# Kernel optimization log

Measured on AMD Instinct MI355X. Metric: run time of the kernel, lower is better.

The kernel has to match this reference:

```python
import jax, jax.numpy as jnp
import numpy as np

N = 512            # hidden_state
BATCH = 64
L = 8192           # seq_len; kernel_max_size == L so kernel length = L
MIN_DELTA = 1e-3
MAX_DELTA = 0.1


def _hippo(n):
    idx = np.arange(n)
    init = np.sqrt(2.0 * idx + 1.0)
    H = np.outer(init, init)           # init @ init.T
    H = np.tril(H)                      # zero strict upper triangle
    H[idx, idx] -= idx                  # diag -= arange(N)
    return (-H).astype(np.float32)


def setup_inputs() -> dict:
    key = jax.random.key(0)
    kx, kb, kc, kd = jax.random.split(key, 4)
    X = jax.random.normal(kx, (BATCH, L), dtype=jnp.float32)
    A = jnp.asarray(_hippo(N))                                   # [N,N] HiPPO init
    Bm = jax.random.normal(kb, (N, 1), dtype=jnp.float32) * (1.0 / N) ** 0.5
    C = jax.random.normal(kc, (1, N), dtype=jnp.float32)
    D = jnp.ones((1,), dtype=jnp.float32)
    log_delta = jax.random.uniform(
        kd, (1,), dtype=jnp.float32,
        minval=np.log(MIN_DELTA), maxval=np.log(MAX_DELTA))
    return {"X": X, "A": A, "Bm": Bm, "C": C, "D": D, "log_delta": log_delta}


def reference(X, A, Bm, C, D, log_delta):
    # delta = exp(clamp(log_delta, log(min), log(max)))
    delta = jnp.exp(jnp.clip(log_delta, jnp.log(MIN_DELTA), jnp.log(MAX_DELTA)))[0]
    # bilinear (Tustin) discretization
    I = jnp.eye(N, dtype=X.dtype)
    A1 = I - delta * 0.5 * A
    A2 = I + delta * 0.5 * A
    Ad = jnp.linalg.solve(A1, A2)           # [N,N]
    Bd = jnp.linalg.solve(A1, delta * Bm)   # [N,1]

    # kernel k[t] = C @ Ad^t @ Bd, t = 0..L-1 (sequential scan)
    def step(v, _):
        return Ad @ v, (C @ v)[0, 0]
    _, k = jax.lax.scan(step, Bd, None, length=L)  # [L]

    # FFT linear (causal) convolution, truncated to L
    end = L + L - 1
    Xd = jnp.fft.rfft(X, n=end, axis=-1)      # [B, F]
    Kd = jnp.fft.rfft(k, n=end)               # [F]
    y = jnp.fft.irfft(Xd * Kd, n=end, axis=-1)[..., :L]
    return y + D * X
```

## Files before the change

kernel.cpp:

```cpp
#include <hip/hip_runtime.h>

#define N 512
#define L 8192

#define LOG_MIN -6.907755278982137f
#define LOG_MAX -2.302585092994046f

typedef __attribute__((ext_vector_type(8))) short short8;
typedef __attribute__((ext_vector_type(4))) float f4;
typedef __attribute__((ext_vector_type(4))) unsigned u4;

__device__ __forceinline__ float get_delta(const float* logd) {
  float ld = logd[0];
  ld = fminf(fmaxf(ld, LOG_MIN), LOG_MAX);
  return expf(ld);
}
__device__ __forceinline__ unsigned short f2bf(float x) {
  union { float f; unsigned int u; } c; c.f = x;
  unsigned int u = c.u;
  u += 0x7FFFu + ((u >> 16) & 1u);
  return (unsigned short)(u >> 16);
}
__device__ __forceinline__ unsigned int pack2(unsigned short a, unsigned short b) {
  return (unsigned int)a | ((unsigned int)b << 16);
}

__device__ __forceinline__ void wts4(float* p, f4 v) {
  asm volatile("global_store_dwordx4 %0, %1, off sc0 sc1"
               :: "v"(p), "v"(v) : "memory");
}
__device__ __forceinline__ void wts4u(unsigned* p, u4 v) {
  asm volatile("global_store_dwordx4 %0, %1, off sc0 sc1"
               :: "v"(p), "v"(v) : "memory");
}
__device__ __forceinline__ void ast(float* p, float v) {
  __hip_atomic_store(p, v, __ATOMIC_RELAXED, __HIP_MEMORY_SCOPE_AGENT);
}

#define NB 152u

__device__ __forceinline__ void gsync(unsigned* bar, int p, int b) {
  asm volatile("s_waitcnt vmcnt(0)" ::: "memory");
  __syncthreads();
  if (threadIdx.x == 0) {
    unsigned* base = bar + p * 128;
    __hip_atomic_fetch_add(base + (b & 7) * 16, 1u, __ATOMIC_RELAXED,
                           __HIP_MEMORY_SCOPE_AGENT);
    unsigned s;
    do {
      s = 0;
#pragma unroll
      for (int i = 0; i < 8; ++i)
        s += __hip_atomic_load(base + i * 16, __ATOMIC_RELAXED,
                               __HIP_MEMORY_SCOPE_AGENT);
      if (s < NB) __builtin_amdgcn_s_sleep(2);
    } while (s < NB);
  }
  __syncthreads();
}


__device__ void diag64(const float* __restrict__ A, float h,
                       float* __restrict__ Xi, int blk, int tid, float* sm) {
  float* Ash = sm;
  float* xs  = sm + 4160;
  float* dinv = sm + 8320;
  int i0 = blk * 64;
  int r = tid >> 2, c0 = (tid & 3) * 16;
#pragma unroll
  for (int q = 0; q < 16; q += 4) {
    f4 v = *(const f4*)(A + (size_t)(i0 + r) * N + i0 + c0 + q);
    Ash[r * 65 + c0 + q] = v.x; Ash[r * 65 + c0 + q + 1] = v.y;
    Ash[r * 65 + c0 + q + 2] = v.z; Ash[r * 65 + c0 + q + 3] = v.w;
  }
  for (int i = tid; i < 4160; i += 256) xs[i] = 0.f;
  __syncthreads();
  if (tid < 64) dinv[tid] = 1.f / (1.f - h * Ash[tid * 65 + tid]);
  __syncthreads();
  int t = tid >> 2, sub = tid & 3;
  for (int rr = 0; rr < 64; ++rr) {
    if (t <= rr) {
      float s = 0.f;
      for (int k = t + sub; k < rr; k += 4) s += Ash[rr * 65 + k] * xs[k * 65 + t];
      s += __shfl_xor(s, 1, 64);
      s += __shfl_xor(s, 2, 64);
      if (sub == 0)
        xs[rr * 65 + t] = (((rr == t) ? 1.f : 0.f) + h * s) * dinv[rr];
    }
  }
  __syncthreads();
#pragma unroll
  for (int q = 0; q < 16; q += 4) {
    f4 v = {xs[r * 65 + c0 + q], xs[r * 65 + c0 + q + 1],
            xs[r * 65 + c0 + q + 2], xs[r * 65 + c0 + q + 3]};
    wts4(Xi + (size_t)(i0 + r) * N + i0 + c0 + q, v);
  }
}

__device__ void lvl64_fused(const float* __restrict__ A, float* __restrict__ Xi,
                            float h, int g, int tid, float* sm) {
  float* X11s = sm;
  float* Us   = sm + 4160;
  int b11 = 128 * g, b22 = 128 * g + 64;
  int r = tid >> 2, c0 = (tid & 3) * 16;
#pragma unroll
  for (int q = 0; q < 16; q += 4) {
    f4 v = *(const f4*)(Xi + (size_t)(b11 + r) * N + b11 + c0 + q);
    X11s[r * 65 + c0 + q] = v.x; X11s[r * 65 + c0 + q + 1] = v.y;
    X11s[r * 65 + c0 + q + 2] = v.z; X11s[r * 65 + c0 + q + 3] = v.w;
  }
  f4 aR[16];
#pragma unroll
  for (int t = 0; t < 16; ++t)
    aR[t] = *(const f4*)(A + (size_t)(b22 + r) * N + b11 + 4 * t);
  __syncthreads();
  float u[16];
#pragma unroll
  for (int j = 0; j < 16; ++j) u[j] = 0.f;
#pragma unroll 4
  for (int k4 = 0; k4 < 16; ++k4) {
    float av[4] = {aR[k4].x, aR[k4].y, aR[k4].z, aR[k4].w};
#pragma unroll
    for (int s = 0; s < 4; ++s) {
      int k = 4 * k4 + s;
      float aa = av[s];
#pragma unroll
      for (int j = 0; j < 16; j += 4) {
        f4 xv = *(const f4*)&X11s[k * 65 + c0 + j];
        u[j] += aa * xv.x; u[j + 1] += aa * xv.y;
        u[j + 2] += aa * xv.z; u[j + 3] += aa * xv.w;
      }
    }
  }
  f4 xR[16];
#pragma unroll
  for (int t = 0; t < 16; ++t)
    xR[t] = *(const f4*)(Xi + (size_t)(b22 + r) * N + b22 + 4 * t);
#pragma unroll
  for (int j = 0; j < 16; ++j) Us[r * 65 + c0 + j] = u[j];
  __syncthreads();
  float x[16];
#pragma unroll
  for (int j = 0; j < 16; ++j) x[j] = 0.f;
#pragma unroll 4
  for (int k4 = 0; k4 < 16; ++k4) {
    float av[4] = {xR[k4].x, xR[k4].y, xR[k4].z, xR[k4].w};
#pragma unroll
    for (int s = 0; s < 4; ++s) {
      int k = 4 * k4 + s;
      float aa = av[s];
#pragma unroll
      for (int j = 0; j < 16; j += 4) {
        f4 xv = *(const f4*)&Us[k * 65 + c0 + j];
        x[j] += aa * xv.x; x[j + 1] += aa * xv.y;
        x[j + 2] += aa * xv.z; x[j + 3] += aa * xv.w;
      }
    }
  }
#pragma unroll
  for (int j = 0; j < 16; j += 4) {
    f4 v = {h * x[j], h * x[j + 1], h * x[j + 2], h * x[j + 3]};
    wts4(&Xi[(size_t)(b22 + r) * N + b11 + c0 + j], v);
  }
}

template <int NT>
__device__ void gemm32t(const float* __restrict__ A_, int lda,
                        const float* __restrict__ B_, int ldb,
                        float* __restrict__ C_, int ldc,
                        int bi, int bj, float alpha, int tid, float* sm) {
  float* As = sm;
  float* Bs = sm + 1056;
  int lr = tid >> 3, lc = (tid & 7) * 4;
  const float* ap = A_ + (size_t)(bi * 32 + lr) * lda + lc;
  const float* bp = B_ + (size_t)lr * ldb + bj * 32 + lc;
  f4 aR[NT], bR[NT];
#pragma unroll
  for (int t = 0; t < NT; ++t) {
    aR[t] = *(const f4*)(ap + 32 * t);
    bR[t] = *(const f4*)(bp + (size_t)(32 * t) * ldb);
  }
  float acc[4] = {0.f, 0.f, 0.f, 0.f};
#pragma unroll
  for (int t = 0; t < NT; ++t) {
    As[lr * 33 + lc] = aR[t].x; As[lr * 33 + lc + 1] = aR[t].y;
    As[lr * 33 + lc + 2] = aR[t].z; As[lr * 33 + lc + 3] = aR[t].w;
    *(f4*)&Bs[lr * 36 + lc] = bR[t];
    __syncthreads();
#pragma unroll
    for (int kk = 0; kk < 32; ++kk) {
      float a = As[lr * 33 + kk];
      f4 bb = *(const f4*)&Bs[kk * 36 + lc];
      acc[0] += a * bb.x; acc[1] += a * bb.y;
      acc[2] += a * bb.z; acc[3] += a * bb.w;
    }
    __syncthreads();
  }
  f4 o = {alpha * acc[0], alpha * acc[1], alpha * acc[2], alpha * acc[3]};
  wts4(&C_[(size_t)(bi * 32 + lr) * ldc + bj * 32 + lc], o);
}

__device__ void sq32(const float* __restrict__ P, float* __restrict__ Q,
                     int bi, int bj, int first, int tid, float* sm) {
  float* As = sm;
  float* Bs = sm + 1056;
  int lr = tid >> 3, lc = (tid & 7) * 4;
  int nk = bi - bj + 1;
  int kb0 = bj * 32;
  int arow = bi * 32 + lr;
  const float* ap = P + (size_t)arow * N + lc;
  const float* bp = P + bj * 32 + lc;
  f4 aR[16], bR[16];
#pragma unroll
  for (int t = 0; t < 16; ++t) {
    if (t < nk) {
      int kt = kb0 + 32 * t;
      aR[t] = *(const f4*)(ap + kt);
      bR[t] = *(const f4*)(bp + (size_t)(kt + lr) * N);
    }
  }
  float acc[4] = {0.f, 0.f, 0.f, 0.f};
#pragma unroll
  for (int t = 0; t < 16; ++t) {
    if (t < nk) {
      int kb = kb0 + 32 * t;
      float a4[4] = {aR[t].x, aR[t].y, aR[t].z, aR[t].w};
      float b4[4] = {bR[t].x, bR[t].y, bR[t].z, bR[t].w};
      if (first) {
#pragma unroll
        for (int j = 0; j < 4; ++j) {
          a4[j] = 2.f * a4[j] - ((arow == kb + lc + j) ? 1.f : 0.f);
          b4[j] = 2.f * b4[j] - ((kb + lr == bj * 32 + lc + j) ? 1.f : 0.f);
        }
      }
      As[lr * 33 + lc] = a4[0]; As[lr * 33 + lc + 1] = a4[1];
      As[lr * 33 + lc + 2] = a4[2]; As[lr * 33 + lc + 3] = a4[3];
      f4 bv = {b4[0], b4[1], b4[2], b4[3]};
      *(f4*)&Bs[lr * 36 + lc] = bv;
      __syncthreads();
#pragma unroll
      for (int kk = 0; kk < 32; ++kk) {
        float a = As[lr * 33 + kk];
        f4 bb = *(const f4*)&Bs[kk * 36 + lc];
        acc[0] += a * bb.x; acc[1] += a * bb.y;
        acc[2] += a * bb.z; acc[3] += a * bb.w;
      }
      __syncthreads();
    }
  }
  f4 o = {acc[0], acc[1], acc[2], acc[3]};
  wts4(&Q[(size_t)(bi * 32 + lr) * N + bj * 32 + lc], o);
}

__device__ void vstep_g(const float* __restrict__ P, float* __restrict__ Vtr,
                        int base, int first, int bi, int tid, float* sm) {
  float* As = sm;
  float* Bs = sm + 1056;
  int lr = tid >> 3, lc = (tid & 7) * 4;
  int cq = tid >> 3, n4 = (tid & 7) * 4;
  int nk = bi + 1;
  const float* ap = P + (size_t)(bi * 32 + lr) * N + lc;
  f4 aR[16];
#pragma unroll
  for (int t = 0; t < 16; ++t)
    if (t < nk) aR[t] = *(const f4*)(ap + 32 * t);
  int ncj = (base > 32) ? 2 : 1;
  for (int cj = 0; cj < ncj; ++cj) {
    int crow = cj * 32 + lr;
    int cok = (crow < base);
    const float* bp = Vtr + (size_t)crow * N + lc;
    f4 bR[16];
#pragma unroll
    for (int t = 0; t < 16; ++t)
      if (t < nk) bR[t] = cok ? *(const f4*)(bp + 32 * t) : (f4){0.f, 0.f, 0.f, 0.f};
    float acc[4] = {0.f, 0.f, 0.f, 0.f};
#pragma unroll
    for (int t = 0; t < 16; ++t) {
      if (t < nk) {
        int kb = 32 * t;
        float a4[4] = {aR[t].x, aR[t].y, aR[t].z, aR[t].w};
        if (first) {
#pragma unroll
          for (int j = 0; j < 4; ++j)
            a4[j] = 2.f * a4[j] - ((bi * 32 + lr == kb + lc + j) ? 1.f : 0.f);
        }
        As[lr * 33 + lc] = a4[0]; As[lr * 33 + lc + 1] = a4[1];
        As[lr * 33 + lc + 2] = a4[2]; As[lr * 33 + lc + 3] = a4[3];
        Bs[lr * 33 + lc] = bR[t].x; Bs[lr * 33 + lc + 1] = bR[t].y;
        Bs[lr * 33 + lc + 2] = bR[t].z; Bs[lr * 33 + lc + 3] = bR[t].w;
        __syncthreads();
#pragma unroll
        for (int kk = 0; kk < 32; ++kk) {
          float b = Bs[cq * 33 + kk];
          acc[0] += As[(n4 + 0) * 33 + kk] * b;
          acc[1] += As[(n4 + 1) * 33 + kk] * b;
          acc[2] += As[(n4 + 2) * 33 + kk] * b;
          acc[3] += As[(n4 + 3) * 33 + kk] * b;
        }
        __syncthreads();
      }
    }
    int c = cj * 32 + cq;
    if (c < base) {
      f4 o = {acc[0], acc[1], acc[2], acc[3]};
      wts4(&Vtr[(size_t)(base + c) * N + bi * 32 + n4], o);
    }
    if (cj + 1 < ncj) __syncthreads();
  }
}

__device__ void wstep_g(const float* __restrict__ P, float* __restrict__ W,
                        int base, int cj, int tid, float* sm) {
  float* As = sm;
  float* Bs = sm + 1056;
  int lr = tid >> 3, lc = (tid & 7) * 4;
  int kb0 = cj * 32, nk = 16 - cj;
  int qok = (lr < base);
  const float* ap = W + (size_t)lr * N + lc;
  const float* bp = P + cj * 32 + lc;
  f4 aR[16], bR[16];
#pragma unroll
  for (int t = 0; t < 16; ++t) {
    if (t < nk) {
      int kt = kb0 + 32 * t;
      aR[t] = qok ? *(const f4*)(ap + kt) : (f4){0.f, 0.f, 0.f, 0.f};
      bR[t] = *(const f4*)(bp + (size_t)(kt + lr) * N);
    }
  }
  float acc[4] = {0.f, 0.f, 0.f, 0.f};
#pragma unroll
  for (int t = 0; t < 16; ++t) {
    if (t < nk) {
      As[lr * 33 + lc] = aR[t].x; As[lr * 33 + lc + 1] = aR[t].y;
      As[lr * 33 + lc + 2] = aR[t].z; As[lr * 33 + lc + 3] = aR[t].w;
      *(f4*)&Bs[lr * 36 + lc] = bR[t];
      __syncthreads();
#pragma unroll
      for (int kk = 0; kk < 32; ++kk) {
        float a = As[lr * 33 + kk];
        f4 bb = *(const f4*)&Bs[kk * 36 + lc];
        acc[0] += a * bb.x; acc[1] += a * bb.y;
        acc[2] += a * bb.z; acc[3] += a * bb.w;
      }
      __syncthreads();
    }
  }
  if (lr < base) {
    f4 o = {acc[0], acc[1], acc[2], acc[3]};
    wts4(&W[(size_t)(base + lr) * N + cj * 32 + lc], o);
  }
}

__device__ void kfinal_g(const float* __restrict__ W, const float* __restrict__ Vtr,
                         float* __restrict__ kvec, int bi, int bj, int tid, float* sm) {
  float* As = sm;
  float* Bs = sm + 1056;
  int lr = tid >> 3, lc = (tid & 7) * 4;
  int q = tid >> 3, r4 = (tid & 7) * 4;
  const float* ap = W + (size_t)(bi * 32 + lr) * N + lc;
  const float* bp = Vtr + (size_t)(bj * 32 + lr) * N + lc;
  f4 aR[16], bR[16];
#pragma unroll
  for (int t = 0; t < 16; ++t) {
    aR[t] = *(const f4*)(ap + 32 * t);
    bR[t] = *(const f4*)(bp + 32 * t);
  }
  float acc[4] = {0.f, 0.f, 0.f, 0.f};
#pragma unroll
  for (int t = 0; t < 16; ++t) {
    As[lr * 33 + lc] = aR[t].x; As[lr * 33 + lc + 1] = aR[t].y;
    As[lr * 33 + lc + 2] = aR[t].z; As[lr * 33 + lc + 3] = aR[t].w;
    Bs[lr * 33 + lc] = bR[t].x; Bs[lr * 33 + lc + 1] = bR[t].y;
    Bs[lr * 33 + lc + 2] = bR[t].z; Bs[lr * 33 + lc + 3] = bR[t].w;
    __syncthreads();
#pragma unroll
    for (int kk = 0; kk < 32; ++kk) {
      float a = As[q * 33 + kk];
      acc[0] += a * Bs[(r4 + 0) * 33 + kk];
      acc[1] += a * Bs[(r4 + 1) * 33 + kk];
      acc[2] += a * Bs[(r4 + 2) * 33 + kk];
      acc[3] += a * Bs[(r4 + 3) * 33 + kk];
    }
    __syncthreads();
  }
  f4 o = {acc[0], acc[1], acc[2], acc[3]};
  wts4(&kvec[(size_t)(bi * 32 + q) * 128 + bj * 32 + r4], o);
}

__device__ void bd1_body(const float* __restrict__ Xi, const float* __restrict__ Bm,
                         float delta, float* __restrict__ Vtr, int bb, int tid,
                         float* sm) {
  float* bs = sm;
  if (tid < 128) ((f4*)bs)[tid] = ((const f4*)Bm)[tid];
  __syncthreads();
  int w = tid >> 6, lane = tid & 63;
#pragma unroll
  for (int pass = 0; pass < 8; ++pass) {
    int row = bb * 32 + w * 8 + pass;
    const float* Xr = Xi + (size_t)row * N + lane * 8;
    f4 a0 = *(const f4*)Xr;
    f4 a1 = *(const f4*)(Xr + 4);
    const float* bp = bs + lane * 8;
    float acc = a0.x * bp[0] + a0.y * bp[1] + a0.z * bp[2] + a0.w * bp[3]
              + a1.x * bp[4] + a1.y * bp[5] + a1.z * bp[6] + a1.w * bp[7];
    acc += __shfl_xor(acc, 1, 64);
    acc += __shfl_xor(acc, 2, 64);
    acc += __shfl_xor(acc, 4, 64);
    acc += __shfl_xor(acc, 8, 64);
    acc += __shfl_xor(acc, 16, 64);
    acc += __shfl_xor(acc, 32, 64);
    if (lane == 0) ast(&Vtr[row], delta * acc);
  }
}

__device__ __forceinline__ void afrag_unit(const float* __restrict__ X,
                                           unsigned* __restrict__ Atab, int u) {
  int lane = u & 63;
  int f = u >> 6;
  int bt = f >> 8, ut = f & 255;
  int row = bt * 16 + (lane & 15);
  int u0 = ut * 32 + ((lane >> 4) << 3);
  const float* xp = X + (size_t)row * L + u0;
  unsigned short v[8];
#pragma unroll
  for (int e = 0; e < 8; ++e) v[e] = f2bf(xp[e]);
  u4 o = {pack2(v[0], v[1]), pack2(v[2], v[3]), pack2(v[4], v[5]), pack2(v[6], v[7])};
  wts4u(Atab + ((size_t)f * 64 + lane) * 4, o);
}

__device__ __forceinline__ void bfrag_unit(const float* __restrict__ kvec,
                                           unsigned* __restrict__ Btab, int u) {
  int lane = u & 63;
  int si = u >> 6;
  int base = si * 16 + (lane & 15) - ((lane >> 4) << 3);
  unsigned short v[8];
#pragma unroll
  for (int e = 0; e < 8; ++e) {
    int idx = base - e;
    float x = (idx >= 0) ? kvec[idx] : 0.0f;
    v[e] = f2bf(x);
  }
  u4 o = {pack2(v[0], v[1]), pack2(v[2], v[3]), pack2(v[4], v[5]), pack2(v[6], v[7])};
  wts4u(Btab + ((size_t)si * 64 + lane) * 4, o);
}

__global__ __launch_bounds__(256) void k_chain(
    const float* __restrict__ A, const float* __restrict__ Bm,
    const float* __restrict__ C, const float* __restrict__ logd,
    const float* __restrict__ X,
    float* __restrict__ Xi, float* __restrict__ U2, float* __restrict__ U3,
    float* __restrict__ PB,
    float* __restrict__ Vtr, float* __restrict__ W, float* __restrict__ kvec,
    unsigned* __restrict__ Atab, unsigned* __restrict__ Btab,
    unsigned* bar) {
  __shared__ float sm[8704];
  int b = blockIdx.x, tid = threadIdx.x;
  float delta = get_delta(logd);
  float h = 0.5f * delta;
#define PBUF(i) (PB + (size_t)(i) * (N * N))
#define GS(p) gsync(bar, (p), b)

  int sbi = 0, srem = b;
  while (srem > sbi) { srem -= (sbi + 1); ++sbi; }
  int sbj = srem;

  if (b < 8) {
    diag64(A, h, Xi, b, tid, sm);
  } else if (b < 36) {
    int idx = b - 8, bi = 0, bj = 0, cnt = 0;
    for (int i = 0; i < 8; ++i)
      for (int j = i + 1; j < 8; ++j) { if (cnt == idx) { bi = i; bj = j; } ++cnt; }
    int r = tid >> 2, c0 = (tid & 3) * 16;
    f4 z = {0.f, 0.f, 0.f, 0.f};
#pragma unroll
    for (int q = 0; q < 16; q += 4)
      wts4(Xi + (size_t)(bi * 64 + r) * N + bj * 64 + c0 + q, z);
  } else if (b == 36) {
    for (int i = tid; i < N; i += 256) ast(&W[i], C[i]);
  } else {
    for (int u = (b - 37) * 256 + tid; u < 65536; u += 115 * 256)
      afrag_unit(X, Atab, u);
  }
  GS(0);
  if (b < 4) lvl64_fused(A, Xi, h, b, tid, sm);
  GS(1);
  if (b < 32) {
    int g = b >> 4, t = b & 15;
    gemm32t<4>(A + (size_t)(256 * g + 128) * N + 256 * g, N,
               Xi + (size_t)(256 * g) * (N + 1), N,
               U2 + g * 16384, 128, t >> 2, t & 3, 1.0f, tid, sm);
  }
  GS(2);
  if (b < 32) {
    int g = b >> 4, t = b & 15;
    gemm32t<4>(Xi + (size_t)(256 * g + 128) * (N + 1), N, U2 + g * 16384, 128,
               Xi + (size_t)(256 * g + 128) * N + 256 * g, N, t >> 2, t & 3, h, tid, sm);
  }
  GS(3);
  if (b < 64)
    gemm32t<8>(A + (size_t)256 * N, N, Xi, N, U3, 256, b >> 3, b & 7, 1.0f, tid, sm);
  GS(4);
  if (b < 64)
    gemm32t<8>(Xi + (size_t)256 * (N + 1), N, U3, 256,
               Xi + (size_t)256 * N, N, b >> 3, b & 7, h, tid, sm);
  GS(5);
  if (b < 136) sq32(Xi, PBUF(0), sbi, sbj, 1, tid, sm);
  else bd1_body(Xi, Bm, delta, Vtr, b - 136, tid, sm);
  GS(6);
  if (b < 136) sq32(PBUF(0), PBUF(1), sbi, sbj, 0, tid, sm);
  else vstep_g(Xi, Vtr, 1, 1, b - 136, tid, sm);
  GS(7);
  if (b < 136) sq32(PBUF(1), PBUF(2), sbi, sbj, 0, tid, sm);
  else vstep_g(PBUF(0), Vtr, 2, 0, b - 136, tid, sm);
  GS(8);
  if (b < 136) sq32(PBUF(2), PBUF(3), sbi, sbj, 0, tid, sm);
  else vstep_g(PBUF(1), Vtr, 4, 0, b - 136, tid, sm);
  GS(9);
  if (b < 136) sq32(PBUF(3), PBUF(4), sbi, sbj, 0, tid, sm);
  else vstep_g(PBUF(2), Vtr, 8, 0, b - 136, tid, sm);
  GS(10);
  if (b < 136) sq32(PBUF(4), PBUF(5), sbi, sbj, 0, tid, sm);
  else vstep_g(PBUF(3), Vtr, 16, 0, b - 136, tid, sm);
  GS(11);
  if (b < 136) sq32(PBUF(5), PBUF(6), sbi, sbj, 0, tid, sm);
  else vstep_g(PBUF(4), Vtr, 32, 0, b - 136, tid, sm);
  GS(12);
  if (b < 136) sq32(PBUF(6), PBUF(7), sbi, sbj, 0, tid, sm);
  else vstep_g(PBUF(5), Vtr, 64, 0, b - 136, tid, sm);
  GS(13);
  if (b < 136) sq32(PBUF(7), PBUF(8), sbi, sbj, 0, tid, sm);
  else wstep_g(PBUF(6), W, 1, b - 136, tid, sm);
  GS(14);
  if (b < 136) sq32(PBUF(8), PBUF(9), sbi, sbj, 0, tid, sm);
  else wstep_g(PBUF(7), W, 2, b - 136, tid, sm);
  GS(15);
  if (b < 136) sq32(PBUF(9), PBUF(10), sbi, sbj, 0, tid, sm);
  else wstep_g(PBUF(8), W, 4, b - 136, tid, sm);
  GS(16);
  if (b < 136) sq32(PBUF(10), PBUF(11), sbi, sbj, 0, tid, sm);
  else wstep_g(PBUF(9), W, 8, b - 136, tid, sm);
  GS(17);
  if (b < 16) wstep_g(PBUF(10), W, 16, b, tid, sm);
  GS(18);
  if (b < 16) wstep_g(PBUF(11), W, 32, b, tid, sm);
  GS(19);
  if (b < 8) kfinal_g(W, Vtr, kvec, b >> 2, b & 3, tid, sm);
  GS(20);
  if (b < 128) bfrag_unit(kvec, Btab, b * 256 + tid);
#undef GS
#undef PBUF
}

__global__ __launch_bounds__(256, 2) void k_convmm(const short8* __restrict__ Atab,
                                                   const short8* __restrict__ Btab,
                                                   const float* __restrict__ X,
                                                   const float* __restrict__ Dp,
                                                   float* __restrict__ Y) {
  __shared__ short8 bsh[32][64];
  int tid = threadIdx.x, lane = tid & 63, bt = tid >> 6;
  int p = blockIdx.x;
  int jL = p, jH = 511 - p;
  int nL = (jL + 2) >> 1, nH = (jH + 2) >> 1;
  f4 aL = {0.f, 0.f, 0.f, 0.f}, aH = {0.f, 0.f, 0.f, 0.f};
  const short8* Abase = Atab + (size_t)bt * 256 * 64 + lane;
  for (int u0 = 0; u0 < nH; u0 += 16) {
#pragma unroll
    for (int k = 0; k < 8; ++k) {
      int idx = tid + 256 * k;
      int f = idx >> 6, ln = idx & 63;
      int i = f & 15;
      int ut = u0 + i;
      if (f < 16) {
        if (ut < nH) bsh[i][ln] = Btab[(size_t)(jH - 2 * ut) * 64 + ln];
      } else {
        if (ut < nL) bsh[16 + i][ln] = Btab[(size_t)(jL - 2 * ut) * 64 + ln];
      }
    }
    __syncthreads();
    int m = (nH - u0 < 16) ? (nH - u0) : 16;
    short8 a = Abase[(size_t)u0 * 64];
    for (int i = 0; i < m; ++i) {
      short8 an;
      if (i + 1 < m) an = Abase[(size_t)(u0 + i + 1) * 64];
      aH = __builtin_amdgcn_mfma_f32_16x16x32_bf16(a, bsh[i][lane], aH, 0, 0, 0);
      if (u0 + i < nL)
        aL = __builtin_amdgcn_mfma_f32_16x16x32_bf16(a, bsh[16 + i][lane], aL, 0, 0, 0);
      a = an;
    }
    __syncthreads();
  }
  float D0 = Dp[0];
  int tt = lane & 15, rq = (lane >> 4) << 2;
#pragma unroll
  for (int r = 0; r < 4; ++r) {
    int bb = bt * 16 + rq + r;
    size_t oL = (size_t)bb * L + jL * 16 + tt;
    size_t oH = (size_t)bb * L + jH * 16 + tt;
    Y[oL] = aL[r] + D0 * X[oL];
    Y[oH] = aH[r] + D0 * X[oH];
  }
}

extern "C" void kernel_launch(void* const* d_in, const int* in_sizes, int n_in,
                              void* d_out, int out_size, void* d_ws, size_t ws_size,
                              hipStream_t stream) {
  const float* X  = (const float*)d_in[0];
  const float* A  = (const float*)d_in[1];
  const float* Bm = (const float*)d_in[2];
  const float* C  = (const float*)d_in[3];
  const float* D  = (const float*)d_in[4];
  const float* ld = (const float*)d_in[5];
  float* Y = (float*)d_out;

  float* ws = (float*)d_ws;
  unsigned* bar = (unsigned*)ws;
  float* kv  = ws + 4096;
  float* Vtr = ws + 12288;
  float* W   = ws + 77824;
  float* Xi  = ws + 110592;
  float* U2  = ws + 372736;
  float* U3  = ws + 405504;
  float* PB  = ws + 471040;
  unsigned* Atab = (unsigned*)(ws + 3616768);
  unsigned* Btab = (unsigned*)(ws + 3878912);

  hipMemsetAsync(bar, 0, 4096 * sizeof(unsigned), stream);
  k_chain<<<152, 256, 0, stream>>>(A, Bm, C, ld, X, Xi, U2, U3, PB, Vtr, W, kv,
                                   Atab, Btab, bar);
  k_convmm<<<256, 256, 0, stream>>>((const short8*)Atab, (const short8*)Btab, X, D, Y);
}
```

Before: 463.6 us.

## Replace persistent grid-barrier chain kernel with a sequence of separate launches

```diff
diff --git a/kernel.cpp b/kernel.cpp
--- a/kernel.cpp
+++ b/kernel.cpp
@@ -25,39 +25,8 @@
   return (unsigned int)a | ((unsigned int)b << 16);
 }
 
-__device__ __forceinline__ void wts4(float* p, f4 v) {
-  asm volatile("global_store_dwordx4 %0, %1, off sc0 sc1"
-               :: "v"(p), "v"(v) : "memory");
-}
-__device__ __forceinline__ void wts4u(unsigned* p, u4 v) {
-  asm volatile("global_store_dwordx4 %0, %1, off sc0 sc1"
-               :: "v"(p), "v"(v) : "memory");
-}
-__device__ __forceinline__ void ast(float* p, float v) {
-  __hip_atomic_store(p, v, __ATOMIC_RELAXED, __HIP_MEMORY_SCOPE_AGENT);
-}
-
-#define NB 152u
-
-__device__ __forceinline__ void gsync(unsigned* bar, int p, int b) {
-  asm volatile("s_waitcnt vmcnt(0)" ::: "memory");
-  __syncthreads();
-  if (threadIdx.x == 0) {
-    unsigned* base = bar + p * 128;
-    __hip_atomic_fetch_add(base + (b & 7) * 16, 1u, __ATOMIC_RELAXED,
-                           __HIP_MEMORY_SCOPE_AGENT);
-    unsigned s;
-    do {
-      s = 0;
-#pragma unroll
-      for (int i = 0; i < 8; ++i)
-        s += __hip_atomic_load(base + i * 16, __ATOMIC_RELAXED,
-                               __HIP_MEMORY_SCOPE_AGENT);
-      if (s < NB) __builtin_amdgcn_s_sleep(2);
-    } while (s < NB);
-  }
-  __syncthreads();
-}
+__device__ __forceinline__ void wts4(float* p, f4 v) { *(f4*)p = v; }
+__device__ __forceinline__ void wts4u(unsigned* p, u4 v) { *(u4*)p = v; }
 
 
 __device__ void diag64(const float* __restrict__ A, float h,
@@ -94,73 +63,6 @@
     f4 v = {xs[r * 65 + c0 + q], xs[r * 65 + c0 + q + 1],
             xs[r * 65 + c0 + q + 2], xs[r * 65 + c0 + q + 3]};
     wts4(Xi + (size_t)(i0 + r) * N + i0 + c0 + q, v);
-  }
-}
-
-__device__ void lvl64_fused(const float* __restrict__ A, float* __restrict__ Xi,
-                            float h, int g, int tid, float* sm) {
-  float* X11s = sm;
-  float* Us   = sm + 4160;
-  int b11 = 128 * g, b22 = 128 * g + 64;
-  int r = tid >> 2, c0 = (tid & 3) * 16;
-#pragma unroll
-  for (int q = 0; q < 16; q += 4) {
-    f4 v = *(const f4*)(Xi + (size_t)(b11 + r) * N + b11 + c0 + q);
-    X11s[r * 65 + c0 + q] = v.x; X11s[r * 65 + c0 + q + 1] = v.y;
-    X11s[r * 65 + c0 + q + 2] = v.z; X11s[r * 65 + c0 + q + 3] = v.w;
-  }
-  f4 aR[16];
-#pragma unroll
-  for (int t = 0; t < 16; ++t)
-    aR[t] = *(const f4*)(A + (size_t)(b22 + r) * N + b11 + 4 * t);
-  __syncthreads();
-  float u[16];
-#pragma unroll
-  for (int j = 0; j < 16; ++j) u[j] = 0.f;
-#pragma unroll 4
-  for (int k4 = 0; k4 < 16; ++k4) {
-    float av[4] = {aR[k4].x, aR[k4].y, aR[k4].z, aR[k4].w};
-#pragma unroll
-    for (int s = 0; s < 4; ++s) {
-      int k = 4 * k4 + s;
-      float aa = av[s];
-#pragma unroll
-      for (int j = 0; j < 16; j += 4) {
-        f4 xv = *(const f4*)&X11s[k * 65 + c0 + j];
-        u[j] += aa * xv.x; u[j + 1] += aa * xv.y;
-        u[j + 2] += aa * xv.z; u[j + 3] += aa * xv.w;
-      }
-    }
-  }
-  f4 xR[16];
-#pragma unroll
-  for (int t = 0; t < 16; ++t)
-    xR[t] = *(const f4*)(Xi + (size_t)(b22 + r) * N + b22 + 4 * t);
-#pragma unroll
-  for (int j = 0; j < 16; ++j) Us[r * 65 + c0 + j] = u[j];
-  __syncthreads();
-  float x[16];
-#pragma unroll
-  for (int j = 0; j < 16; ++j) x[j] = 0.f;
-#pragma unroll 4
-  for (int k4 = 0; k4 < 16; ++k4) {
-    float av[4] = {xR[k4].x, xR[k4].y, xR[k4].z, xR[k4].w};
-#pragma unroll
-    for (int s = 0; s < 4; ++s) {
-      int k = 4 * k4 + s;
-      float aa = av[s];
-#pragma unroll
-      for (int j = 0; j < 16; j += 4) {
-        f4 xv = *(const f4*)&Us[k * 65 + c0 + j];
-        x[j] += aa * xv.x; x[j + 1] += aa * xv.y;
-        x[j + 2] += aa * xv.z; x[j + 3] += aa * xv.w;
-      }
-    }
-  }
-#pragma unroll
-  for (int j = 0; j < 16; j += 4) {
-    f4 v = {h * x[j], h * x[j + 1], h * x[j + 2], h * x[j + 3]};
-    wts4(&Xi[(size_t)(b22 + r) * N + b11 + c0 + j], v);
   }
 }
 
@@ -409,7 +311,7 @@
     acc += __shfl_xor(acc, 8, 64);
     acc += __shfl_xor(acc, 16, 64);
     acc += __shfl_xor(acc, 32, 64);
-    if (lane == 0) ast(&Vtr[row], delta * acc);
+    if (lane == 0) Vtr[row] = delta * acc;
   }
 }
 
@@ -444,28 +346,24 @@
   wts4u(Btab + ((size_t)si * 64 + lane) * 4, o);
 }
 
-__global__ __launch_bounds__(256) void k_chain(
-    const float* __restrict__ A, const float* __restrict__ Bm,
-    const float* __restrict__ C, const float* __restrict__ logd,
-    const float* __restrict__ X,
-    float* __restrict__ Xi, float* __restrict__ U2, float* __restrict__ U3,
-    float* __restrict__ PB,
-    float* __restrict__ Vtr, float* __restrict__ W, float* __restrict__ kvec,
-    unsigned* __restrict__ Atab, unsigned* __restrict__ Btab,
-    unsigned* bar) {
-  __shared__ float sm[8704];
-  int b = blockIdx.x, tid = threadIdx.x;
-  float delta = get_delta(logd);
-  float h = 0.5f * delta;
-#define PBUF(i) (PB + (size_t)(i) * (N * N))
-#define GS(p) gsync(bar, (p), b)
-
+__device__ __forceinline__ void tridec(int b, int& bi, int& bj) {
   int sbi = 0, srem = b;
   while (srem > sbi) { srem -= (sbi + 1); ++sbi; }
-  int sbj = srem;
-
+  bi = sbi; bj = srem;
+}
+
+
+__global__ __launch_bounds__(256) void k_p0(const float* __restrict__ A,
+                                            const float* __restrict__ C,
+                                            const float* __restrict__ logd,
+                                            const float* __restrict__ X,
+                                            float* __restrict__ Xi,
+                                            float* __restrict__ W,
+                                            unsigned* __restrict__ Atab) {
+  __shared__ float sm[8448];
+  int b = blockIdx.x, tid = threadIdx.x;
   if (b < 8) {
-    diag64(A, h, Xi, b, tid, sm);
+    diag64(A, 0.5f * get_delta(logd), Xi, b, tid, sm);
   } else if (b < 36) {
     int idx = b - 8, bi = 0, bj = 0, cnt = 0;
     for (int i = 0; i < 8; ++i)
@@ -476,79 +374,182 @@
     for (int q = 0; q < 16; q += 4)
       wts4(Xi + (size_t)(bi * 64 + r) * N + bj * 64 + c0 + q, z);
   } else if (b == 36) {
-    for (int i = tid; i < N; i += 256) ast(&W[i], C[i]);
+    for (int i = tid; i < N; i += 256) W[i] = C[i];
   } else {
     for (int u = (b - 37) * 256 + tid; u < 65536; u += 115 * 256)
       afrag_unit(X, Atab, u);
   }
-  GS(0);
-  if (b < 4) lvl64_fused(A, Xi, h, b, tid, sm);
-  GS(1);
-  if (b < 32) {
-    int g = b >> 4, t = b & 15;
-    gemm32t<4>(A + (size_t)(256 * g + 128) * N + 256 * g, N,
-               Xi + (size_t)(256 * g) * (N + 1), N,
-               U2 + g * 16384, 128, t >> 2, t & 3, 1.0f, tid, sm);
-  }
-  GS(2);
-  if (b < 32) {
-    int g = b >> 4, t = b & 15;
-    gemm32t<4>(Xi + (size_t)(256 * g + 128) * (N + 1), N, U2 + g * 16384, 128,
-               Xi + (size_t)(256 * g + 128) * N + 256 * g, N, t >> 2, t & 3, h, tid, sm);
-  }
-  GS(3);
-  if (b < 64)
-    gemm32t<8>(A + (size_t)256 * N, N, Xi, N, U3, 256, b >> 3, b & 7, 1.0f, tid, sm);
-  GS(4);
-  if (b < 64)
-    gemm32t<8>(Xi + (size_t)256 * (N + 1), N, U3, 256,
-               Xi + (size_t)256 * N, N, b >> 3, b & 7, h, tid, sm);
-  GS(5);
-  if (b < 136) sq32(Xi, PBUF(0), sbi, sbj, 1, tid, sm);
-  else bd1_body(Xi, Bm, delta, Vtr, b - 136, tid, sm);
-  GS(6);
-  if (b < 136) sq32(PBUF(0), PBUF(1), sbi, sbj, 0, tid, sm);
-  else vstep_g(Xi, Vtr, 1, 1, b - 136, tid, sm);
-  GS(7);
-  if (b < 136) sq32(PBUF(1), PBUF(2), sbi, sbj, 0, tid, sm);
-  else vstep_g(PBUF(0), Vtr, 2, 0, b - 136, tid, sm);
-  GS(8);
-  if (b < 136) sq32(PBUF(2), PBUF(3), sbi, sbj, 0, tid, sm);
-  else vstep_g(PBUF(1), Vtr, 4, 0, b - 136, tid, sm);
-  GS(9);
-  if (b < 136) sq32(PBUF(3), PBUF(4), sbi, sbj, 0, tid, sm);
-  else vstep_g(PBUF(2), Vtr, 8, 0, b - 136, tid, sm);
-  GS(10);
-  if (b < 136) sq32(PBUF(4), PBUF(5), sbi, sbj, 0, tid, sm);
-  else vstep_g(PBUF(3), Vtr, 16, 0, b - 136, tid, sm);
-  GS(11);
-  if (b < 136) sq32(PBUF(5), PBUF(6), sbi, sbj, 0, tid, sm);
-  else vstep_g(PBUF(4), Vtr, 32, 0, b - 136, tid, sm);
-  GS(12);
-  if (b < 136) sq32(PBUF(6), PBUF(7), sbi, sbj, 0, tid, sm);
-  else vstep_g(PBUF(5), Vtr, 64, 0, b - 136, tid, sm);
-  GS(13);
-  if (b < 136) sq32(PBUF(7), PBUF(8), sbi, sbj, 0, tid, sm);
-  else wstep_g(PBUF(6), W, 1, b - 136, tid, sm);
-  GS(14);
-  if (b < 136) sq32(PBUF(8), PBUF(9), sbi, sbj, 0, tid, sm);
-  else wstep_g(PBUF(7), W, 2, b - 136, tid, sm);
-  GS(15);
-  if (b < 136) sq32(PBUF(9), PBUF(10), sbi, sbj, 0, tid, sm);
-  else wstep_g(PBUF(8), W, 4, b - 136, tid, sm);
-  GS(16);
-  if (b < 136) sq32(PBUF(10), PBUF(11), sbi, sbj, 0, tid, sm);
-  else wstep_g(PBUF(9), W, 8, b - 136, tid, sm);
-  GS(17);
-  if (b < 16) wstep_g(PBUF(10), W, 16, b, tid, sm);
-  GS(18);
-  if (b < 16) wstep_g(PBUF(11), W, 32, b, tid, sm);
-  GS(19);
-  if (b < 8) kfinal_g(W, Vtr, kvec, b >> 2, b & 3, tid, sm);
-  GS(20);
-  if (b < 128) bfrag_unit(kvec, Btab, b * 256 + tid);
-#undef GS
-#undef PBUF
+}
+
+__global__ __launch_bounds__(256) void k_lvl64(const float* __restrict__ A,
+                                               const float* __restrict__ logd,
+                                               float* __restrict__ Xi) {
+  __shared__ float sm[8448];
+  float* X11s = sm;
+  float* Us = sm + 4160;
+  float h = 0.5f * get_delta(logd);
+  int g = blockIdx.x, tid = threadIdx.x;
+  int b11 = 128 * g, b22 = 128 * g + 64;
+  int r = tid >> 2, c0 = (tid & 3) * 16;
+#pragma unroll
+  for (int q = 0; q < 16; q += 4) {
+    f4 v = *(const f4*)(Xi + (size_t)(b11 + r) * N + b11 + c0 + q);
+    X11s[r * 65 + c0 + q] = v.x; X11s[r * 65 + c0 + q + 1] = v.y;
+    X11s[r * 65 + c0 + q + 2] = v.z; X11s[r * 65 + c0 + q + 3] = v.w;
+  }
+  f4 aR[16];
+#pragma unroll
+  for (int t = 0; t < 16; ++t)
+    aR[t] = *(const f4*)(A + (size_t)(b22 + r) * N + b11 + 4 * t);
+  __syncthreads();
+  float u[16];
+#pragma unroll
+  for (int j = 0; j < 16; ++j) u[j] = 0.f;
+#pragma unroll 4
+  for (int k4 = 0; k4 < 16; ++k4) {
+    float av[4] = {aR[k4].x, aR[k4].y, aR[k4].z, aR[k4].w};
+#pragma unroll
+    for (int s = 0; s < 4; ++s) {
+      int k = 4 * k4 + s;
+      float aa = av[s];
+#pragma unroll
+      for (int j = 0; j < 16; j += 4) {
+        f4 xv = *(const f4*)&X11s[k * 65 + c0 + j];
+        u[j] += aa * xv.x; u[j + 1] += aa * xv.y;
+        u[j + 2] += aa * xv.z; u[j + 3] += aa * xv.w;
+      }
+    }
+  }
+  f4 xR[16];
+#pragma unroll
+  for (int t = 0; t < 16; ++t)
+    xR[t] = *(const f4*)(Xi + (size_t)(b22 + r) * N + b22 + 4 * t);
+#pragma unroll
+  for (int j = 0; j < 16; ++j) Us[r * 65 + c0 + j] = u[j];
+  __syncthreads();
+  float x[16];
+#pragma unroll
+  for (int j = 0; j < 16; ++j) x[j] = 0.f;
+#pragma unroll 4
+  for (int k4 = 0; k4 < 16; ++k4) {
+    float av[4] = {xR[k4].x, xR[k4].y, xR[k4].z, xR[k4].w};
+#pragma unroll
+    for (int s = 0; s < 4; ++s) {
+      int k = 4 * k4 + s;
+      float aa = av[s];
+#pragma unroll
+      for (int j = 0; j < 16; j += 4) {
+        f4 xv = *(const f4*)&Us[k * 65 + c0 + j];
+        x[j] += aa * xv.x; x[j + 1] += aa * xv.y;
+        x[j + 2] += aa * xv.z; x[j + 3] += aa * xv.w;
+      }
+    }
+  }
+#pragma unroll
+  for (int j = 0; j < 16; j += 4) {
+    f4 v = {h * x[j], h * x[j + 1], h * x[j + 2], h * x[j + 3]};
+    wts4(&Xi[(size_t)(b22 + r) * N + b11 + c0 + j], v);
+  }
+}
+
+__global__ __launch_bounds__(256) void k_triA(const float* __restrict__ A,
+                                              const float* __restrict__ Xi,
+                                              float* __restrict__ U2) {
+  __shared__ float sm[2304];
+  int b = blockIdx.x, tid = threadIdx.x;
+  int g = b >> 4, t = b & 15;
+  gemm32t<4>(A + (size_t)(256 * g + 128) * N + 256 * g, N,
+             Xi + (size_t)(256 * g) * (N + 1), N,
+             U2 + g * 16384, 128, t >> 2, t & 3, 1.0f, tid, sm);
+}
+__global__ __launch_bounds__(256) void k_triB(const float* __restrict__ logd,
+                                              float* __restrict__ Xi,
+                                              const float* __restrict__ U2) {
+  __shared__ float sm[2304];
+  int b = blockIdx.x, tid = threadIdx.x;
+  int g = b >> 4, t = b & 15;
+  float h = 0.5f * get_delta(logd);
+  gemm32t<4>(Xi + (size_t)(256 * g + 128) * (N + 1), N, U2 + g * 16384, 128,
+             Xi + (size_t)(256 * g + 128) * N + 256 * g, N, t >> 2, t & 3, h, tid, sm);
+}
+__global__ __launch_bounds__(256) void k_triC(const float* __restrict__ A,
+                                              const float* __restrict__ Xi,
+                                              float* __restrict__ U3) {
+  __shared__ float sm[2304];
+  int b = blockIdx.x, tid = threadIdx.x;
+  gemm32t<8>(A + (size_t)256 * N, N, Xi, N, U3, 256, b >> 3, b & 7, 1.0f, tid, sm);
+}
+__global__ __launch_bounds__(256) void k_triD(const float* __restrict__ logd,
+                                              float* __restrict__ Xi,
+                                              const float* __restrict__ U3) {
+  __shared__ float sm[2304];
+  int b = blockIdx.x, tid = threadIdx.x;
+  float h = 0.5f * get_delta(logd);
+  gemm32t<8>(Xi + (size_t)256 * (N + 1), N, U3, 256,
+             Xi + (size_t)256 * N, N, b >> 3, b & 7, h, tid, sm);
+}
+
+__global__ __launch_bounds__(256) void k_sqbd(const float* __restrict__ Xi,
+                                              float* __restrict__ Q,
+                                              const float* __restrict__ Bm,
+                                              const float* __restrict__ logd,
+                                              float* __restrict__ Vtr) {
+  __shared__ float sm[2304];
+  int b = blockIdx.x, tid = threadIdx.x;
+  if (b < 136) {
+    int bi, bj; tridec(b, bi, bj);
+    sq32(Xi, Q, bi, bj, 1, tid, sm);
+  } else {
+    bd1_body(Xi, Bm, get_delta(logd), Vtr, b - 136, tid, sm);
+  }
+}
+
+__global__ __launch_bounds__(256) void k_sqv(const float* __restrict__ P,
+                                             float* __restrict__ Q,
+                                             const float* __restrict__ Pv,
+                                             float* __restrict__ Vtr,
+                                             int base, int first) {
+  __shared__ float sm[2304];
+  int b = blockIdx.x, tid = threadIdx.x;
+  if (b < 136) {
+    int bi, bj; tridec(b, bi, bj);
+    sq32(P, Q, bi, bj, 0, tid, sm);
+  } else {
+    vstep_g(Pv, Vtr, base, first, b - 136, tid, sm);
+  }
+}
+
+__global__ __launch_bounds__(256) void k_sqw(const float* __restrict__ P,
+                                             float* __restrict__ Q,
+                                             const float* __restrict__ Pw,
+                                             float* __restrict__ W,
+                                             int base) {
+  __shared__ float sm[2304];
+  int b = blockIdx.x, tid = threadIdx.x;
+  if (b < 136) {
+    int bi, bj; tridec(b, bi, bj);
+    sq32(P, Q, bi, bj, 0, tid, sm);
+  } else {
+    wstep_g(Pw, W, base, b - 136, tid, sm);
+  }
+}
+
+__global__ __launch_bounds__(256) void k_wf(const float* __restrict__ Pw,
+                                            float* __restrict__ W, int base) {
+  __shared__ float sm[2304];
+  wstep_g(Pw, W, base, blockIdx.x, threadIdx.x, sm);
+}
+
+__global__ __launch_bounds__(256) void k_kf(const float* __restrict__ W,
+                                            const float* __restrict__ Vtr,
+                                            float* __restrict__ kvec) {
+  __shared__ float sm[2304];
+  kfinal_g(W, Vtr, kvec, blockIdx.x >> 2, blockIdx.x & 3, threadIdx.x, sm);
+}
+
+__global__ __launch_bounds__(256) void k_bf(const float* __restrict__ kvec,
+                                            unsigned* __restrict__ Btab) {
+  bfrag_unit(kvec, Btab, blockIdx.x * 256 + threadIdx.x);
 }
 
 __global__ __launch_bounds__(256, 2) void k_convmm(const short8* __restrict__ Atab,
@@ -613,19 +614,40 @@
   float* Y = (float*)d_out;
 
   float* ws = (float*)d_ws;
-  unsigned* bar = (unsigned*)ws;
-  float* kv  = ws + 4096;
-  float* Vtr = ws + 12288;
-  float* W   = ws + 77824;
-  float* Xi  = ws + 110592;
-  float* U2  = ws + 372736;
-  float* U3  = ws + 405504;
-  float* PB  = ws + 471040;
-  unsigned* Atab = (unsigned*)(ws + 3616768);
-  unsigned* Btab = (unsigned*)(ws + 3878912);
-
-  hipMemsetAsync(bar, 0, 4096 * sizeof(unsigned), stream);
-  k_chain<<<152, 256, 0, stream>>>(A, Bm, C, ld, X, Xi, U2, U3, PB, Vtr, W, kv,
-                                   Atab, Btab, bar);
+  float* kv  = ws;
+  float* Vtr = ws + 8192;
+  float* W   = ws + 73728;
+  float* Xi  = ws + 106496;
+  float* U2  = ws + 368640;
+  float* U3  = ws + 401408;
+  float* PB  = ws + 466944;
+  unsigned* Atab = (unsigned*)(ws + 3612672);
+  unsigned* Btab = (unsigned*)(ws + 3874816);
+#define PBUF(i) (PB + (size_t)(i) * (N * N))
+
+  k_p0<<<152, 256, 0, stream>>>(A, C, ld, X, Xi, W, Atab);
+  k_lvl64<<<4, 256, 0, stream>>>(A, ld, Xi);
+  k_triA<<<32, 256, 0, stream>>>(A, Xi, U2);
+  k_triB<<<32, 256, 0, stream>>>(ld, Xi, U2);
+  k_triC<<<64, 256, 0, stream>>>(A, Xi, U3);
+  k_triD<<<64, 256, 0, stream>>>(ld, Xi, U3);
+
+  k_sqbd<<<152, 256, 0, stream>>>(Xi, PBUF(0), Bm, ld, Vtr);
+  k_sqv<<<152, 256, 0, stream>>>(PBUF(0), PBUF(1), Xi, Vtr, 1, 1);
+  k_sqv<<<152, 256, 0, stream>>>(PBUF(1), PBUF(2), PBUF(0), Vtr, 2, 0);
+  k_sqv<<<152, 256, 0, stream>>>(PBUF(2), PBUF(3), PBUF(1), Vtr, 4, 0);
+  k_sqv<<<152, 256, 0, stream>>>(PBUF(3), PBUF(4), PBUF(2), Vtr, 8, 0);
+  k_sqv<<<152, 256, 0, stream>>>(PBUF(4), PBUF(5), PBUF(3), Vtr, 16, 0);
+  k_sqv<<<152, 256, 0, stream>>>(PBUF(5), PBUF(6), PBUF(4), Vtr, 32, 0);
+  k_sqv<<<152, 256, 0, stream>>>(PBUF(6), PBUF(7), PBUF(5), Vtr, 64, 0);
+  k_sqw<<<152, 256, 0, stream>>>(PBUF(7), PBUF(8), PBUF(6), W, 1);
+  k_sqw<<<152, 256, 0, stream>>>(PBUF(8), PBUF(9), PBUF(7), W, 2);
+  k_sqw<<<152, 256, 0, stream>>>(PBUF(9), PBUF(10), PBUF(8), W, 4);
+  k_sqw<<<152, 256, 0, stream>>>(PBUF(10), PBUF(11), PBUF(9), W, 8);
+  k_wf<<<16, 256, 0, stream>>>(PBUF(10), W, 16);
+  k_wf<<<16, 256, 0, stream>>>(PBUF(11), W, 32);
+  k_kf<<<8, 256, 0, stream>>>(W, Vtr, kv);
+  k_bf<<<128, 256, 0, stream>>>(kv, Btab);
   k_convmm<<<256, 256, 0, stream>>>((const short8*)Atab, (const short8*)Btab, X, D, Y);
-}
+#undef PBUF
+}
```

Result: slower. 556.1 us (+20.0%).

## Restructure Toeplitz conv matmul: split K across wave pairs, drop LDS staging

Applied to the files above, without the earlier changes.

```diff
diff --git a/kernel.cpp b/kernel.cpp
--- a/kernel.cpp
+++ b/kernel.cpp
@@ -551,53 +551,48 @@
 #undef PBUF
 }
 
-__global__ __launch_bounds__(256, 2) void k_convmm(const short8* __restrict__ Atab,
-                                                   const short8* __restrict__ Btab,
-                                                   const float* __restrict__ X,
-                                                   const float* __restrict__ Dp,
-                                                   float* __restrict__ Y) {
-  __shared__ short8 bsh[32][64];
-  int tid = threadIdx.x, lane = tid & 63, bt = tid >> 6;
-  int p = blockIdx.x;
-  int jL = p, jH = 511 - p;
-  int nL = (jL + 2) >> 1, nH = (jH + 2) >> 1;
-  f4 aL = {0.f, 0.f, 0.f, 0.f}, aH = {0.f, 0.f, 0.f, 0.f};
-  const short8* Abase = Atab + (size_t)bt * 256 * 64 + lane;
-  for (int u0 = 0; u0 < nH; u0 += 16) {
-#pragma unroll
-    for (int k = 0; k < 8; ++k) {
-      int idx = tid + 256 * k;
-      int f = idx >> 6, ln = idx & 63;
-      int i = f & 15;
-      int ut = u0 + i;
-      if (f < 16) {
-        if (ut < nH) bsh[i][ln] = Btab[(size_t)(jH - 2 * ut) * 64 + ln];
-      } else {
-        if (ut < nL) bsh[16 + i][ln] = Btab[(size_t)(jL - 2 * ut) * 64 + ln];
-      }
-    }
-    __syncthreads();
-    int m = (nH - u0 < 16) ? (nH - u0) : 16;
-    short8 a = Abase[(size_t)u0 * 64];
-    for (int i = 0; i < m; ++i) {
-      short8 an;
-      if (i + 1 < m) an = Abase[(size_t)(u0 + i + 1) * 64];
-      aH = __builtin_amdgcn_mfma_f32_16x16x32_bf16(a, bsh[i][lane], aH, 0, 0, 0);
-      if (u0 + i < nL)
-        aL = __builtin_amdgcn_mfma_f32_16x16x32_bf16(a, bsh[16 + i][lane], aL, 0, 0, 0);
-      a = an;
-    }
-    __syncthreads();
-  }
-  float D0 = Dp[0];
-  int tt = lane & 15, rq = (lane >> 4) << 2;
-#pragma unroll
-  for (int r = 0; r < 4; ++r) {
-    int bb = bt * 16 + rq + r;
-    size_t oL = (size_t)bb * L + jL * 16 + tt;
-    size_t oH = (size_t)bb * L + jH * 16 + tt;
-    Y[oL] = aL[r] + D0 * X[oL];
-    Y[oH] = aH[r] + D0 * X[oH];
+__global__ __launch_bounds__(512) void k_convmm(const short8* __restrict__ Atab,
+                                                const short8* __restrict__ Btab,
+                                                const float* __restrict__ X,
+                                                const float* __restrict__ Dp,
+                                                float* __restrict__ Y) {
+  int tid = threadIdx.x;
+  int lane = tid & 63;
+  int w = tid >> 6;
+  int bt = w & 3;
+  int kh = w >> 2;
+  int blk = blockIdx.x;
+  int t0 = blk * 32;
+  int nsteps = blk + 1;
+  f4 acc0 = {0.f, 0.f, 0.f, 0.f};
+  f4 acc1 = {0.f, 0.f, 0.f, 0.f};
+  for (int ut = kh; ut < nsteps; ut += 2) {
+    short8 a = Atab[(size_t)(bt * 256 + ut) * 64 + lane];
+    int si0 = 2 * (blk - ut);
+    short8 b0 = Btab[(size_t)si0 * 64 + lane];
+    short8 b1 = Btab[(size_t)(si0 + 1) * 64 + lane];
+    acc0 = __builtin_amdgcn_mfma_f32_16x16x32_bf16(a, b0, acc0, 0, 0, 0);
+    acc1 = __builtin_amdgcn_mfma_f32_16x16x32_bf16(a, b1, acc1, 0, 0, 0);
+  }
+  __shared__ float red[4][64][8];
+  if (kh == 1) {
+#pragma unroll
+    for (int r = 0; r < 4; ++r) {
+      red[bt][lane][r] = acc0[r];
+      red[bt][lane][4 + r] = acc1[r];
+    }
+  }
+  __syncthreads();
+  if (kh == 0) {
+    float D0 = Dp[0];
+#pragma unroll
+    for (int r = 0; r < 4; ++r) {
+      int bb = bt * 16 + ((lane >> 4) << 2) + r;
+      int t = t0 + (lane & 15);
+      size_t o0 = (size_t)bb * L + t;
+      Y[o0] = acc0[r] + red[bt][lane][r] + D0 * X[o0];
+      Y[o0 + 16] = acc1[r] + red[bt][lane][4 + r] + D0 * X[o0 + 16];
+    }
   }
 }
 
@@ -627,5 +622,5 @@
   hipMemsetAsync(bar, 0, 4096 * sizeof(unsigned), stream);
   k_chain<<<152, 256, 0, stream>>>(A, Bm, C, ld, X, Xi, U2, U3, PB, Vtr, W, kv,
                                    Atab, Btab, bar);
-  k_convmm<<<256, 256, 0, stream>>>((const short8*)Atab, (const short8*)Btab, X, D, Y);
-}
+  k_convmm<<<256, 512, 0, stream>>>((const short8*)Atab, (const short8*)Btab, X, D, Y);
+}
```

Result: faster. 416.7 us (-10.1%).
